# Optimization experiments

Hardware: AMD Instinct MI355X
Metric: run time of the kernel (lower is better)

The kernel has to match this reference:

```python
import jax, jax.numpy as jnp
import numpy as np

KERNEL = 5
OUT_CAPS = 8
OUT_ATOMS = 32
ROUTINGS = 3


def _squash(x):
    # squash nonlinearity: (|v|^2 / (1+|v|^2)) * v/|v|, over last (atom) axis
    norm = jnp.linalg.norm(x, axis=-1, keepdims=True)
    norm_sq = norm * norm
    return (x / norm) * (norm_sq / (1.0 + norm_sq))


def setup_inputs() -> dict:
    key = jax.random.key(0)
    k1, k2, k3 = jax.random.split(key, 3)
    B, H, Wd, inC, inA = 16, 32, 32, 8, 16
    inputs = jax.random.normal(k1, (B, H, Wd, inC, inA), dtype=jnp.float32)
    # He-normal-ish conv kernel [k, k, inA, outC*outA]
    fan_in = KERNEL * KERNEL * inA
    W = jax.random.normal(k2, (KERNEL, KERNEL, inA, OUT_CAPS * OUT_ATOMS), dtype=jnp.float32) * np.sqrt(2.0 / fan_in)
    b = jnp.full((1, 1, OUT_CAPS, OUT_ATOMS), 0.1, dtype=jnp.float32)
    return {"inputs": inputs, "W": W, "b": b}


def reference(inputs, W, b):
    B, H, Wd, inC, inA = inputs.shape
    # transpose to [inC, B, H, W, inA] and fold capsules into batch for shared conv
    x = jnp.transpose(inputs, (3, 0, 1, 2, 4)).reshape(inC * B, H, Wd, inA)
    conv = jax.lax.conv_general_dilated(
        x, W, window_strides=(1, 1), padding="SAME",
        dimension_numbers=("NHWC", "HWIO", "NHWC"))
    Hp, Wp = conv.shape[1], conv.shape[2]
    # faithful to original TF reshape (row-major) of [inC*B,...] -> [B, inC, ...]
    votes = conv.reshape(B, inC, Hp, Wp, OUT_CAPS, OUT_ATOMS)
    biases = jnp.broadcast_to(b, (Hp, Wp, OUT_CAPS, OUT_ATOMS))

    logits = jnp.zeros((B, inC, Hp, Wp, OUT_CAPS), dtype=votes.dtype)
    act = None
    for _ in range(ROUTINGS):
        route = jax.nn.softmax(logits, axis=-1)  # over output capsules
        # weighted sum of votes over input capsules: [B, Hp, Wp, outC, outA]
        preact = jnp.einsum("bihwc,bihwca->bhwca", route, votes) + biases
        act = _squash(preact)
        # agreement: dot(votes, activation) over atoms -> logit update
        logits = logits + jnp.sum(votes * act[:, None], axis=-1)
    return act
```

## Files before the change

### kernel.cpp

```cpp
#include <hip/hip_runtime.h>


typedef __attribute__((ext_vector_type(2))) _Float16 f16x2;
typedef __attribute__((ext_vector_type(8))) _Float16 f16x8;
typedef __attribute__((ext_vector_type(16))) float f32x16;

union f16x8u { f16x8 v; f16x2 d[4]; unsigned short s[8]; unsigned int u32[4]; unsigned long long u[2]; };
union f16x2u { f16x2 v; unsigned int u; unsigned short s[2]; };

__device__ __forceinline__ unsigned short f2h(float x) {
  union { _Float16 h; unsigned short u; } v;
  v.h = (_Float16)x;
  return v.u;
}

__global__ __launch_bounds__(256) void wprep_kernel(
    const float* __restrict__ W, unsigned short* __restrict__ wsh) {
  int t = blockIdx.x * 256 + threadIdx.x;
  int khkw = t >> 12;
  int rem  = t & 4095;
  int ch = rem >> 4, ia = rem & 15;
  wsh[t] = f2h(W[khkw * 4096 + ia * 256 + ch]);
}

__global__ __launch_bounds__(256, 2) void capsconv_mfma_kernel(
    const float* __restrict__ inp,
    const unsigned short* __restrict__ wsh,
    const float* __restrict__ bias,
    float* __restrict__ out)
{
  __shared__ char smem[21120];
  const _Float16* wshh = (const _Float16*)wsh;
  float* logitL = (float*)(smem + 19456);
  float* scaleL = (float*)(smem + 20992);

  const int tid  = threadIdx.x;
  const int wid  = tid >> 6;
  const int lane = tid & 63;
  const int sub  = lane >> 5;
  const int ln31 = lane & 31;

  const int bid = blockIdx.x;
  const int wq = bid & 7;
  const int h  = (bid >> 3) & 31;
  const int bb = bid >> 8;
  const int i_src  = bb >> 1;
  const int b_base = (bb & 1) * 8;

  #pragma unroll
  for (int s = 0; s < 5; ++s) {
    int e = tid + s * 256;
    int kh  = e >> 8;
    int ii  = (e >> 5) & 7;
    int wl  = (e >> 2) & 7;
    int iaq = e & 3;
    int hh = h + kh - 2;
    int wsrc = wq * 4 + wl - 2;
    float4 v = make_float4(0.f, 0.f, 0.f, 0.f);
    if ((unsigned)hh < 32u && (unsigned)wsrc < 32u)
      v = *(const float4*)(inp +
          ((((size_t)(b_base + ii) * 32 + hh) * 32 + wsrc) * 8 + i_src) * 16 + iaq * 4);
    union { _Float16 hx[4]; unsigned long long u; } pkk;
    pkk.hx[0] = (_Float16)v.x; pkk.hx[1] = (_Float16)v.y;
    pkk.hx[2] = (_Float16)v.z; pkk.hx[3] = (_Float16)v.w;
    *(unsigned long long*)(smem + kh * 2176 + ii * 272 + wl * 32 + iaq * 8) = pkk.u;
  }
  __syncthreads();

  f32x16 acc[2];
  #pragma unroll
  for (int nt = 0; nt < 2; ++nt)
    #pragma unroll
    for (int e = 0; e < 16; ++e) acc[nt][e] = 0.f;

  const char* aBase = smem + (ln31 & 7) * 272 + (ln31 >> 3) * 32 + sub * 16;
  const _Float16* bBase = wshh + (wid * 64 + ln31) * 16 + sub * 8;

  #pragma unroll
  for (int kh = 0; kh < 5; ++kh) {
    f16x8 af[5], bf0[5], bf1[5];
    #pragma unroll
    for (int kw = 0; kw < 5; ++kw) {
      af[kw]  = *(const f16x8*)(aBase + kh * 2176 + kw * 32);
      bf0[kw] = *(const f16x8*)(bBase + (size_t)(kh * 5 + kw) * 4096);
      bf1[kw] = *(const f16x8*)(bBase + (size_t)(kh * 5 + kw) * 4096 + 512);
    }
    #pragma unroll
    for (int kw = 0; kw < 5; ++kw) {
      acc[0] = __builtin_amdgcn_mfma_f32_32x32x16_f16(af[kw], bf0[kw], acc[0], 0, 0, 0);
      acc[1] = __builtin_amdgcn_mfma_f32_32x32x16_f16(af[kw], bf1[kw], acc[1], 0, 0, 0);
    }
  }

  unsigned int pk[2][4][2];
  #pragma unroll
  for (int nt = 0; nt < 2; ++nt)
    #pragma unroll
    for (int w = 0; w < 4; ++w) {
      f16x2u lo, hi;
      lo.v = f16x2{(_Float16)acc[nt][w * 4 + 0], (_Float16)acc[nt][w * 4 + 1]};
      hi.v = f16x2{(_Float16)acc[nt][w * 4 + 2], (_Float16)acc[nt][w * 4 + 3]};
      pk[nt][w][0] = lo.u; pk[nt][w][1] = hi.u;
    }
  f16x8 vreg[4];
  #pragma unroll
  for (int w = 0; w < 4; ++w) {
    unsigned int own0 = sub ? pk[1][w][0] : pk[0][w][0];
    unsigned int own1 = sub ? pk[1][w][1] : pk[0][w][1];
    unsigned int snd0 = sub ? pk[0][w][0] : pk[1][w][0];
    unsigned int snd1 = sub ? pk[0][w][1] : pk[1][w][1];
    unsigned int rc0 = (unsigned int)__shfl_xor((int)snd0, 32, 64);
    unsigned int rc1 = (unsigned int)__shfl_xor((int)snd1, 32, 64);
    f16x8u vv;
    vv.u32[0] = sub ? rc0 : own0;
    vv.u32[1] = sub ? rc1 : own1;
    vv.u32[2] = sub ? own0 : rc0;
    vv.u32[3] = sub ? own1 : rc1;
    vreg[w] = vv.v;
  }

  __syncthreads();
  {
    const int cT = (tid >> 5) & 7, qT = (tid >> 3) & 3, aT = tid & 7;
    #pragma unroll
    for (int w = 0; w < 4; ++w) {
      f16x8u vv; vv.v = vreg[w];
      #pragma unroll
      for (int ii = 0; ii < 8; ++ii) {
        int bp = qT * 8 + (((cT + qT) & 7) ^ ii);
        *(unsigned short*)(smem + w * 4352 + ii * 544 + bp * 16 + aT * 2) = vv.s[ii];
      }
    }
  }
  ((unsigned short*)(smem + 20480))[tid] = 0x3000;
  __syncthreads();

  const int c_t = (tid >> 5) & 7;
  const int q_t = (tid >> 3) & 3;
  const int a_t = tid & 7;
  const float bv = bias[tid];
  const int aw  = tid >> 6;
  const int aii = (tid >> 3) & 7;
  const int ac  = tid & 7;

  float pre[4];
  #pragma unroll 1
  for (int rt = 0; rt < 3; ++rt) {
    if (rt > 0) {
      if (tid < 32) {
        int wv = tid >> 3, ii = tid & 7;
        float l[8];
        #pragma unroll
        for (int c = 0; c < 8; ++c) l[c] = logitL[(wv * 8 + ii) * 8 + c];
        float mx = fmaxf(fmaxf(fmaxf(l[0], l[1]), fmaxf(l[2], l[3])),
                         fmaxf(fmaxf(l[4], l[5]), fmaxf(l[6], l[7])));
        float den = 0.f;
        #pragma unroll
        for (int c = 0; c < 8; ++c) den += __expf(l[c] - mx);
        float inv = 1.f / den;
        #pragma unroll
        for (int c = 0; c < 8; ++c)
          ((unsigned short*)(smem + 20480))[(wv * 8 + c) * 8 + ii] =
              f2h(__expf(l[c] - mx) * inv);
      }
      __syncthreads();
    }
    #pragma unroll
    for (int w = 0; w < 4; ++w) {
      f16x8u rp, vv;
      rp.v = *(const f16x8*)(smem + 20480 + ((w * 8 + c_t) * 8) * 2);
      vv.v = vreg[w];
      float p = bv;
      #pragma unroll
      for (int d = 0; d < 4; ++d)
        p = __builtin_amdgcn_fdot2(vv.d[d], rp.d[d], p, false);
      pre[w] = p;
      *(unsigned short*)(smem + 17408 + w * 512 + q_t * 128 + c_t * 16 + a_t * 2) = f2h(p);
    }
    __syncthreads();
    if (tid < 32) {
      int wv = tid >> 3, cc = tid & 7;
      const char* pp = smem + 17408 + wv * 512 + cc * 16;
      f16x8u x0, x1, x2, x3;
      x0.v = *(const f16x8*)(pp);
      x1.v = *(const f16x8*)(pp + 128);
      x2.v = *(const f16x8*)(pp + 256);
      x3.v = *(const f16x8*)(pp + 384);
      float n0 = 0.f, n1 = 0.f, n2 = 0.f, n3 = 0.f;
      #pragma unroll
      for (int d = 0; d < 4; ++d) {
        n0 = __builtin_amdgcn_fdot2(x0.d[d], x0.d[d], n0, false);
        n1 = __builtin_amdgcn_fdot2(x1.d[d], x1.d[d], n1, false);
        n2 = __builtin_amdgcn_fdot2(x2.d[d], x2.d[d], n2, false);
        n3 = __builtin_amdgcn_fdot2(x3.d[d], x3.d[d], n3, false);
      }
      float nsq = (n0 + n1) + (n2 + n3);
      scaleL[tid] = sqrtf(nsq) / (1.f + nsq);
    }
    __syncthreads();
    if (rt < 2) {
      float dot = 0.f;
      #pragma unroll
      for (int q = 0; q < 4; ++q) {
        f16x8u vv, aa;
        vv.v = *(const f16x8*)(smem + aw * 4352 + aii * 544 +
                               (q * 8 + (((ac + q) & 7) ^ aii)) * 16);
        aa.v = *(const f16x8*)(smem + 17408 + aw * 512 + q * 128 + ac * 16);
        #pragma unroll
        for (int d = 0; d < 4; ++d)
          dot = __builtin_amdgcn_fdot2(vv.d[d], aa.d[d], dot, false);
      }
      float ds = dot * scaleL[aw * 8 + ac];
      int idx = (aw * 8 + aii) * 8 + ac;
      if (rt == 0) logitL[idx] = ds;
      else         logitL[idx] += ds;
      __syncthreads();
    } else {
      #pragma unroll
      for (int w = 0; w < 4; ++w)
        out[((size_t)((bb * 32 + h) * 32 + wq * 4 + w)) * 256 + tid] =
            pre[w] * scaleL[w * 8 + c_t];
    }
  }
}

extern "C" void kernel_launch(void* const* d_in, const int* in_sizes, int n_in,
                              void* d_out, int out_size, void* d_ws, size_t ws_size,
                              hipStream_t stream) {
  (void)in_sizes; (void)n_in; (void)ws_size; (void)out_size;
  const float* inp  = (const float*)d_in[0];
  const float* W    = (const float*)d_in[1];
  const float* bv   = (const float*)d_in[2];
  float* out        = (float*)d_out;
  unsigned short* wsh = (unsigned short*)d_ws;

  hipLaunchKernelGGL(wprep_kernel, dim3(400), dim3(256), 0, stream, W, wsh);
  hipLaunchKernelGGL(capsconv_mfma_kernel, dim3(4096), dim3(256), 0, stream,
                     inp, wsh, bv, out);
}
```

Measured before the change: 54.89 us.

## Move routing loop to per-wave register/shuffle reductions, removing block barriers

Rewrites the dynamic-routing phase so each wavefront owns one output pixel. It holds that pixel's votes in fp32 registers and does the softmax, squash norm and agreement reductions with lane shuffles instead of shared-memory round trips and block-wide __syncthreads. This removes the fp16 staging of preactivations and logits and most of the barriers, and it shrinks LDS use. In exchange it costs more registers, which may reduce occupancy, and adds many cross-lane shuffle operations.

After: 57.91 us. 1.05x slower.

```diff
diff --git a/kernel.cpp b/kernel.cpp
--- a/kernel.cpp
+++ b/kernel.cpp
@@ -29,10 +29,8 @@
     const float* __restrict__ bias,
     float* __restrict__ out)
 {
-  __shared__ char smem[21120];
+  __shared__ char smem[17408];
   const _Float16* wshh = (const _Float16*)wsh;
-  float* logitL = (float*)(smem + 19456);
-  float* scaleL = (float*)(smem + 20992);
 
   const int tid  = threadIdx.x;
   const int wid  = tid >> 6;
@@ -120,108 +118,85 @@
   }
 
   __syncthreads();
-  {
-    const int cT = (tid >> 5) & 7, qT = (tid >> 3) & 3, aT = tid & 7;
-    #pragma unroll
-    for (int w = 0; w < 4; ++w) {
-      f16x8u vv; vv.v = vreg[w];
+  #pragma unroll
+  for (int w = 0; w < 4; ++w)
+    *(f16x8*)(smem + w * 4352 + (tid >> 2) * 68 + (tid & 3) * 16) = vreg[w];
+  __syncthreads();
+
+  const int k = lane & 7;
+  float vv[4][8];
+  #pragma unroll
+  for (int j = 0; j < 4; ++j) {
+    f16x8u t8;
+    t8.v = *(const f16x8*)(smem + wid * 4352 + lane * 68 + j * 16);
+    #pragma unroll
+    for (int ii = 0; ii < 8; ++ii) vv[j][ii] = (float)t8.v[ii];
+  }
+  const float4 bv4 = *(const float4*)(bias + lane * 4);
+  const float bvj[4] = {bv4.x, bv4.y, bv4.z, bv4.w};
+
+  float logit_k = 0.f;
+  float pre[4], scale = 0.f;
+
+  #pragma unroll
+  for (int rt = 0; rt < 3; ++rt) {
+    float r[8];
+    if (rt == 0) {
+      #pragma unroll
+      for (int i = 0; i < 8; ++i) r[i] = 0.125f;
+    } else {
+      float mx = logit_k;
+      mx = fmaxf(mx, __shfl_xor(mx, 8, 64));
+      mx = fmaxf(mx, __shfl_xor(mx, 16, 64));
+      mx = fmaxf(mx, __shfl_xor(mx, 32, 64));
+      float e = __expf(logit_k - mx);
+      float den = e;
+      den += __shfl_xor(den, 8, 64);
+      den += __shfl_xor(den, 16, 64);
+      den += __shfl_xor(den, 32, 64);
+      float route_k = e / den;
+      int cbase = lane & 56;
+      #pragma unroll
+      for (int i = 0; i < 8; ++i) r[i] = __shfl(route_k, cbase | i, 64);
+    }
+    #pragma unroll
+    for (int j = 0; j < 4; ++j) {
+      float p = bvj[j];
+      #pragma unroll
+      for (int ii = 0; ii < 8; ++ii) p = fmaf(r[ii], vv[j][ii], p);
+      pre[j] = p;
+    }
+    float nsq = pre[0] * pre[0] + pre[1] * pre[1] + pre[2] * pre[2] + pre[3] * pre[3];
+    nsq += __shfl_xor(nsq, 1, 64);
+    nsq += __shfl_xor(nsq, 2, 64);
+    nsq += __shfl_xor(nsq, 4, 64);
+    scale = sqrtf(nsq) / (1.f + nsq);
+    if (rt < 2) {
+      float dot8[8];
       #pragma unroll
       for (int ii = 0; ii < 8; ++ii) {
-        int bp = qT * 8 + (((cT + qT) & 7) ^ ii);
-        *(unsigned short*)(smem + w * 4352 + ii * 544 + bp * 16 + aT * 2) = vv.s[ii];
+        float d = vv[0][ii] * pre[0];
+        d = fmaf(vv[1][ii], pre[1], d);
+        d = fmaf(vv[2][ii], pre[2], d);
+        d = fmaf(vv[3][ii], pre[3], d);
+        d += __shfl_xor(d, 1, 64);
+        d += __shfl_xor(d, 2, 64);
+        d += __shfl_xor(d, 4, 64);
+        dot8[ii] = d;
       }
-    }
-  }
-  ((unsigned short*)(smem + 20480))[tid] = 0x3000;
-  __syncthreads();
-
-  const int c_t = (tid >> 5) & 7;
-  const int q_t = (tid >> 3) & 3;
-  const int a_t = tid & 7;
-  const float bv = bias[tid];
-  const int aw  = tid >> 6;
-  const int aii = (tid >> 3) & 7;
-  const int ac  = tid & 7;
-
-  float pre[4];
-  #pragma unroll 1
-  for (int rt = 0; rt < 3; ++rt) {
-    if (rt > 0) {
-      if (tid < 32) {
-        int wv = tid >> 3, ii = tid & 7;
-        float l[8];
-        #pragma unroll
-        for (int c = 0; c < 8; ++c) l[c] = logitL[(wv * 8 + ii) * 8 + c];
-        float mx = fmaxf(fmaxf(fmaxf(l[0], l[1]), fmaxf(l[2], l[3])),
-                         fmaxf(fmaxf(l[4], l[5]), fmaxf(l[6], l[7])));
-        float den = 0.f;
-        #pragma unroll
-        for (int c = 0; c < 8; ++c) den += __expf(l[c] - mx);
-        float inv = 1.f / den;
-        #pragma unroll
-        for (int c = 0; c < 8; ++c)
-          ((unsigned short*)(smem + 20480))[(wv * 8 + c) * 8 + ii] =
-              f2h(__expf(l[c] - mx) * inv);
-      }
-      __syncthreads();
-    }
-    #pragma unroll
-    for (int w = 0; w < 4; ++w) {
-      f16x8u rp, vv;
-      rp.v = *(const f16x8*)(smem + 20480 + ((w * 8 + c_t) * 8) * 2);
-      vv.v = vreg[w];
-      float p = bv;
-      #pragma unroll
-      for (int d = 0; d < 4; ++d)
-        p = __builtin_amdgcn_fdot2(vv.d[d], rp.d[d], p, false);
-      pre[w] = p;
-      *(unsigned short*)(smem + 17408 + w * 512 + q_t * 128 + c_t * 16 + a_t * 2) = f2h(p);
-    }
-    __syncthreads();
-    if (tid < 32) {
-      int wv = tid >> 3, cc = tid & 7;
-      const char* pp = smem + 17408 + wv * 512 + cc * 16;
-      f16x8u x0, x1, x2, x3;
-      x0.v = *(const f16x8*)(pp);
-      x1.v = *(const f16x8*)(pp + 128);
-      x2.v = *(const f16x8*)(pp + 256);
-      x3.v = *(const f16x8*)(pp + 384);
-      float n0 = 0.f, n1 = 0.f, n2 = 0.f, n3 = 0.f;
-      #pragma unroll
-      for (int d = 0; d < 4; ++d) {
-        n0 = __builtin_amdgcn_fdot2(x0.d[d], x0.d[d], n0, false);
-        n1 = __builtin_amdgcn_fdot2(x1.d[d], x1.d[d], n1, false);
-        n2 = __builtin_amdgcn_fdot2(x2.d[d], x2.d[d], n2, false);
-        n3 = __builtin_amdgcn_fdot2(x3.d[d], x3.d[d], n3, false);
-      }
-      float nsq = (n0 + n1) + (n2 + n3);
-      scaleL[tid] = sqrtf(nsq) / (1.f + nsq);
-    }
-    __syncthreads();
-    if (rt < 2) {
-      float dot = 0.f;
-      #pragma unroll
-      for (int q = 0; q < 4; ++q) {
-        f16x8u vv, aa;
-        vv.v = *(const f16x8*)(smem + aw * 4352 + aii * 544 +
-                               (q * 8 + (((ac + q) & 7) ^ aii)) * 16);
-        aa.v = *(const f16x8*)(smem + 17408 + aw * 512 + q * 128 + ac * 16);
-        #pragma unroll
-        for (int d = 0; d < 4; ++d)
-          dot = __builtin_amdgcn_fdot2(vv.d[d], aa.d[d], dot, false);
-      }
-      float ds = dot * scaleL[aw * 8 + ac];
-      int idx = (aw * 8 + aii) * 8 + ac;
-      if (rt == 0) logitL[idx] = ds;
-      else         logitL[idx] += ds;
-      __syncthreads();
-    } else {
-      #pragma unroll
-      for (int w = 0; w < 4; ++w)
-        out[((size_t)((bb * 32 + h) * 32 + wq * 4 + w)) * 256 + tid] =
-            pre[w] * scaleL[w * 8 + c_t];
-    }
-  }
+      bool b0 = (k & 1), b1 = (k & 2), b2 = (k & 4);
+      float e0 = b0 ? dot8[1] : dot8[0];
+      float e1 = b0 ? dot8[3] : dot8[2];
+      float e2 = b0 ? dot8[5] : dot8[4];
+      float e3 = b0 ? dot8[7] : dot8[6];
+      float f0 = b1 ? e1 : e0;
+      float f1 = b1 ? e3 : e2;
+      logit_k = fmaf(scale, b2 ? f1 : f0, logit_k);
+    }
+  }
+  const size_t pos = (size_t)((bb * 32 + h) * 32 + wq * 4 + wid);
+  float4 o = make_float4(pre[0] * scale, pre[1] * scale, pre[2] * scale, pre[3] * scale);
+  *(float4*)(out + pos * 256 + lane * 4) = o;
 }
 
 extern "C" void kernel_launch(void* const* d_in, const int* in_sizes, int n_in,
```
